# Optimization experiments

Measured on AMD Instinct MI355X. Metric: run time of the kernel, lower is better.

## Reference

```python
import jax, jax.numpy as jnp
from jax import lax
import numpy as np

DIM = 768
NUM_HEADS = 12
HEAD_DIM = DIM // NUM_HEADS
POOL = 8
LAM1_INIT = 0.5
LAM2_INIT = 0.5
EPS = 1e-6


def rmsnorm(x, w):
    # x / (||x||_2 / sqrt(d) + eps) * w
    d = x.shape[-1]
    rms = jnp.sqrt(jnp.sum(x * x, axis=-1, keepdims=True)) / jnp.sqrt(jnp.asarray(d, x.dtype))
    return x / (rms + EPS) * w


def setup_inputs() -> dict:
    key = jax.random.key(0)
    ks = jax.random.split(key, 10)
    B, H, W = 32, 32, 32
    N = H * W
    x = jax.random.normal(ks[0], (B, N, DIM), dtype=jnp.float32)
    Wqkv = jax.random.normal(ks[1], (3 * DIM, DIM), dtype=jnp.float32) * 0.02
    Wproj = jax.random.normal(ks[2], (DIM, DIM), dtype=jnp.float32) * 0.02
    bproj = jnp.zeros((DIM,), dtype=jnp.float32)
    Wpos = jax.random.normal(ks[3], (HEAD_DIM, HEAD_DIM), dtype=jnp.float32) * 0.02
    Wneg = jax.random.normal(ks[4], (HEAD_DIM, HEAD_DIM), dtype=jnp.float32) * 0.02
    conv_w = jax.random.normal(ks[5], (HEAD_DIM, 1, 3, 3), dtype=jnp.float32) * 0.1  # depthwise OIHW
    lam1 = jnp.asarray(LAM1_INIT, dtype=jnp.float32)
    lam2 = jnp.asarray(LAM2_INIT, dtype=jnp.float32)
    norm1_w = jnp.ones((HEAD_DIM,), dtype=jnp.float32)
    norm2_w = jnp.ones((HEAD_DIM,), dtype=jnp.float32)
    return {"x": x, "Wqkv": Wqkv, "Wproj": Wproj, "bproj": bproj, "Wpos": Wpos,
            "Wneg": Wneg, "conv_w": conv_w, "lam1": lam1, "lam2": lam2,
            "norm1_w": norm1_w, "norm2_w": norm2_w, "H": H, "W": W}


def reference(x, Wqkv, Wproj, bproj, Wpos, Wneg, conv_w, lam1, lam2, norm1_w, norm2_w, H, W):
    B, N, C = x.shape
    h, hd, p = NUM_HEADS, HEAD_DIM, POOL
    scale = hd ** -0.5
    # qkv projection -> [3, B, h, N, hd]
    qkv = (x @ Wqkv.T).reshape(B, N, 3, h, hd).transpose(2, 0, 3, 1, 4)
    q, k, v = qkv[0], qkv[1], qkv[2]
    # depthwise conv + GELU on q in spatial form
    q2 = q.reshape(B, h, H, W, hd).transpose(0, 1, 4, 2, 3).reshape(B * h, hd, H, W)
    qe = lax.conv_general_dilated(q2, conv_w, window_strides=(1, 1), padding='SAME',
                                  feature_group_count=hd,
                                  dimension_numbers=('NCHW', 'OIHW', 'NCHW'))
    qe = jax.nn.gelu(qe, approximate=False)
    # adaptive avg pool to (p, p): exact since H % p == 0
    qp = qe.reshape(B * h, hd, p, H // p, p, W // p).mean(axis=(3, 5))
    t_base = qp.reshape(B, h, hd, p, p).transpose(0, 1, 3, 4, 2).reshape(B, h, p * p, hd)
    # dynamic e+/e- embeddings from global query
    gq = q.mean(axis=2)  # [B, h, hd]
    t_pos = t_base + (gq @ Wpos.T)[:, :, None, :]
    t_neg = t_base + (gq @ Wneg.T)[:, :, None, :]
    # stage 1: pooled contrast tokens attend to k/v
    attn_pos = jax.nn.softmax(jnp.einsum('bhmd,bhnd->bhmn', t_pos, k) * scale, axis=-1)
    v_hat_pos = attn_pos @ v  # [B, h, p*p, hd]
    attn_neg = jax.nn.softmax(jnp.einsum('bhmd,bhnd->bhmn', t_neg, k) * scale, axis=-1)
    v_hat_neg = attn_neg @ v
    v_contrast = rmsnorm(v_hat_pos - lam1 * v_hat_neg, norm1_w) * (1.0 - LAM1_INIT)
    # stage 2: q attends to contrast tokens
    attn1 = jax.nn.softmax(jnp.einsum('bhnd,bhmd->bhnm', q, t_pos) * scale, axis=-1)
    attn2 = jax.nn.softmax(jnp.einsum('bhnd,bhmd->bhnm', q, t_neg) * scale, axis=-1)
    out_patch = (attn1 - lam2 * attn2) @ v_contrast  # [B, h, N, hd]
    out_patch = rmsnorm(out_patch, norm2_w) * (1.0 - LAM2_INIT)
    out_patch = out_patch.transpose(0, 2, 1, 3).reshape(B, N, C)
    out = out_patch @ Wproj.T + bproj
    return out
```

## Files before the change

kernel.cpp:

```cpp
#include <hip/hip_runtime.h>
#include <hip/hip_bf16.h>


typedef __attribute__((ext_vector_type(8))) short short8;
typedef __attribute__((ext_vector_type(4))) short bf16x4;
typedef __attribute__((ext_vector_type(4))) float f32x4;

#define DEV static __device__ __forceinline__

DEV unsigned short f2bf(float f) {
  unsigned int b; __builtin_memcpy(&b, &f, 4);
  unsigned int r = (b + 0x7FFFu + ((b >> 16) & 1u)) >> 16;
  return (unsigned short)r;
}
DEV float bf2f(unsigned short u) {
  unsigned int b = ((unsigned int)u) << 16;
  float f; __builtin_memcpy(&f, &b, 4);
  return f;
}

DEV void gload16(const unsigned short* g, unsigned short* l) {
  __builtin_amdgcn_global_load_lds(
      (const __attribute__((address_space(1))) unsigned int*)g,
      (__attribute__((address_space(3))) unsigned int*)l, 16, 0, 0);
}

DEV void bar() {
  asm volatile("" ::: "memory");
  __builtin_amdgcn_s_barrier();
  asm volatile("" ::: "memory");
}
DEV void wait_vm4() { asm volatile("s_waitcnt vmcnt(4)" ::: "memory"); __builtin_amdgcn_sched_barrier(0); }
DEV void wait_vm0() { asm volatile("s_waitcnt vmcnt(0)" ::: "memory"); __builtin_amdgcn_sched_barrier(0); }
DEV void wait_lgkm0() { asm volatile("s_waitcnt lgkmcnt(0)" ::: "memory"); __builtin_amdgcn_sched_barrier(0); }

constexpr size_t SZ_QKV = (size_t)32 * 12 * 1024 * 64 * 2;
constexpr size_t OFF_Q   = 0;
constexpr size_t OFF_K   = OFF_Q + SZ_QKV;
constexpr size_t OFF_VT  = OFF_K + SZ_QKV;
constexpr size_t OFF_TPB = OFF_VT + SZ_QKV;
constexpr size_t OFF_TNB = OFF_TPB + 3145728;
constexpr size_t OFF_VCT = OFF_TNB + 3145728;
constexpr size_t OFF_OP  = OFF_VCT + 6291456;
constexpr size_t OFF_XB  = OFF_OP + SZ_QKV;
constexpr size_t OFF_WQ  = OFF_XB + SZ_QKV;
constexpr size_t OFF_WP  = OFF_WQ + 3538944;
constexpr size_t OFF_EP  = OFF_WP + 1179648;
constexpr size_t OFF_EN  = OFF_EP + 98304;

__global__ __launch_bounds__(256) void cast3_kernel(const float* __restrict__ x,
    const float* __restrict__ wq, const float* __restrict__ wp,
    unsigned short* __restrict__ xd, unsigned short* __restrict__ wqd,
    unsigned short* __restrict__ wpd) {
  const int i = blockIdx.x * 256 + threadIdx.x;
  const float* src; unsigned short* dst; int off;
  if (i < 6291456) { src = x; dst = xd; off = i; }
  else if (i < 6733824) { src = wq; dst = wqd; off = i - 6291456; }
  else { src = wp; dst = wpd; off = i - 6733824; }
  float4 v = reinterpret_cast<const float4*>(src)[off];
  ushort4 o;
  o.x = f2bf(v.x); o.y = f2bf(v.y); o.z = f2bf(v.z); o.w = f2bf(v.w);
  reinterpret_cast<ushort4*>(dst)[off] = o;
}

DEV void stage_ht(const unsigned short* __restrict__ G, unsigned short* shbase,
                  int grow0, int k0, int htrow0, int w, int lane) {
  const int rl = lane >> 3;
  const int ck = (lane & 7) ^ rl;
  const unsigned short* s0 = G + (size_t)(grow0 + htrow0 + w * 16 + rl) * 768 + k0 + ck * 8;
  gload16(s0, shbase + (htrow0 + w * 16) * 64);
  gload16(s0 + (size_t)8 * 768, shbase + (htrow0 + w * 16 + 8) * 64);
}

__global__ __launch_bounds__(512, 2) void gemm_qkv_kernel(const unsigned short* __restrict__ A,
    const unsigned short* __restrict__ Bm, unsigned short* __restrict__ q,
    unsigned short* __restrict__ k, unsigned short* __restrict__ vt) {
  __shared__ __align__(16) unsigned short sh[65536];
  const int t = threadIdx.x;
  const int lane = t & 63;
  const int w = t >> 6;
  const int wm = w >> 2, wn = w & 3;
  const int l = lane & 15, g = lane >> 4;
  const int id = blockIdx.x;
  const int swz = (id & 7) * 144 + (id >> 3);
  const int rt = swz / 9, ct = swz % 9;
  const int row0 = rt * 256, col0 = ct * 256;

  f32x4 acc[8][4];
#pragma unroll
  for (int i = 0; i < 8; ++i)
#pragma unroll
    for (int j = 0; j < 4; ++j) acc[i][j] = (f32x4){0.f, 0.f, 0.f, 0.f};

  stage_ht(A, sh, row0, 0, 0, w, lane);
  stage_ht(A, sh, row0, 0, 128, w, lane);
  stage_ht(Bm, sh + 32768, col0, 0, 0, w, lane);
  stage_ht(Bm, sh + 32768, col0, 0, 128, w, lane);
  stage_ht(Bm, sh + 32768 + 16384, col0, 64, 0, w, lane);
  stage_ht(Bm, sh + 32768 + 16384, col0, 64, 128, w, lane);
  wait_vm4();
  bar();

  for (int m = 0; m < 12; ++m) {
    const int d = m & 1;
    const unsigned short* Ab = sh + d * 16384;
    const unsigned short* Bb = sh + 32768 + d * 16384;
    short8 af[4][2], bf0[2][2], bf1[2][2];
#pragma unroll
    for (int mt = 0; mt < 4; ++mt)
#pragma unroll
      for (int kc = 0; kc < 2; ++kc) {
        const int r = wm * 128 + mt * 16 + l;
        af[mt][kc] = *reinterpret_cast<const short8*>(Ab + r * 64 + (((kc << 2) | g) ^ (r & 7)) * 8);
      }
#pragma unroll
    for (int nt = 0; nt < 2; ++nt)
#pragma unroll
      for (int kc = 0; kc < 2; ++kc) {
        const int r = wn * 64 + nt * 16 + l;
        bf0[nt][kc] = *reinterpret_cast<const short8*>(Bb + r * 64 + (((kc << 2) | g) ^ (r & 7)) * 8);
      }
    if (m + 1 < 12) stage_ht(A, sh + (d ^ 1) * 16384, row0, (m + 1) * 64, 0, w, lane);
    bar();
    __builtin_amdgcn_s_setprio(1);
#pragma unroll
    for (int kc = 0; kc < 2; ++kc)
#pragma unroll
      for (int mt = 0; mt < 4; ++mt)
#pragma unroll
        for (int nt = 0; nt < 2; ++nt)
          acc[mt][nt] = __builtin_amdgcn_mfma_f32_16x16x32_bf16(af[mt][kc], bf0[nt][kc], acc[mt][nt], 0, 0, 0);
    __builtin_amdgcn_s_setprio(0);
    bar();
#pragma unroll
    for (int nt = 0; nt < 2; ++nt)
#pragma unroll
      for (int kc = 0; kc < 2; ++kc) {
        const int r = wn * 64 + 32 + nt * 16 + l;
        bf1[nt][kc] = *reinterpret_cast<const short8*>(Bb + r * 64 + (((kc << 2) | g) ^ (r & 7)) * 8);
      }
    if (m + 1 < 12) stage_ht(A, sh + (d ^ 1) * 16384, row0, (m + 1) * 64, 128, w, lane);
    bar();
    __builtin_amdgcn_s_setprio(1);
#pragma unroll
    for (int kc = 0; kc < 2; ++kc)
#pragma unroll
      for (int mt = 0; mt < 4; ++mt)
#pragma unroll
        for (int nt = 0; nt < 2; ++nt)
          acc[mt][2 + nt] = __builtin_amdgcn_mfma_f32_16x16x32_bf16(af[mt][kc], bf1[nt][kc], acc[mt][2 + nt], 0, 0, 0);
    __builtin_amdgcn_s_setprio(0);
    bar();
#pragma unroll
    for (int mt = 0; mt < 4; ++mt)
#pragma unroll
      for (int kc = 0; kc < 2; ++kc) {
        const int r = wm * 128 + 64 + mt * 16 + l;
        af[mt][kc] = *reinterpret_cast<const short8*>(Ab + r * 64 + (((kc << 2) | g) ^ (r & 7)) * 8);
      }
    if (m + 2 < 12) stage_ht(Bm, sh + 32768 + d * 16384, col0, (m + 2) * 64, 0, w, lane);
    bar();
    __builtin_amdgcn_s_setprio(1);
#pragma unroll
    for (int kc = 0; kc < 2; ++kc)
#pragma unroll
      for (int mt = 0; mt < 4; ++mt)
#pragma unroll
        for (int nt = 0; nt < 2; ++nt)
          acc[4 + mt][2 + nt] = __builtin_amdgcn_mfma_f32_16x16x32_bf16(af[mt][kc], bf1[nt][kc], acc[4 + mt][2 + nt], 0, 0, 0);
    __builtin_amdgcn_s_setprio(0);
    bar();
    if (m + 2 < 12) stage_ht(Bm, sh + 32768 + d * 16384, col0, (m + 2) * 64, 128, w, lane);
    bar();
    __builtin_amdgcn_s_setprio(1);
#pragma unroll
    for (int kc = 0; kc < 2; ++kc)
#pragma unroll
      for (int mt = 0; mt < 4; ++mt)
#pragma unroll
        for (int nt = 0; nt < 2; ++nt)
          acc[4 + mt][nt] = __builtin_amdgcn_mfma_f32_16x16x32_bf16(af[mt][kc], bf0[nt][kc], acc[4 + mt][nt], 0, 0, 0);
    __builtin_amdgcn_s_setprio(0);
    if (m < 11) {
      if (m == 10) wait_vm0(); else wait_vm4();
    }
    bar();
  }

  const int s_ = ct / 3;
  if (s_ == 2) {
#pragma unroll
    for (int ni = 0; ni < 4; ++ni) {
      const int colg = (ct % 3) * 256 + wn * 64 + ni * 16 + l;
      const int head = colg >> 6, dd = colg & 63;
#pragma unroll
      for (int mi = 0; mi < 8; ++mi) {
        const int row = row0 + wm * 128 + mi * 16 + (g << 2);
        const int b = row >> 10, n = row & 1023;
        ushort4 pk;
        pk.x = f2bf(acc[mi][ni][0]); pk.y = f2bf(acc[mi][ni][1]);
        pk.z = f2bf(acc[mi][ni][2]); pk.w = f2bf(acc[mi][ni][3]);
        *reinterpret_cast<ushort4*>(vt + ((((size_t)b * 12 + head) * 64 + dd) << 10) + n) = pk;
      }
    }
  } else {
    unsigned short* dst = (s_ == 0) ? q : k;
#pragma unroll
    for (int ni = 0; ni < 4; ++ni) {
      const int colg = (ct % 3) * 256 + wn * 64 + ni * 16 + l;
      const int head = colg >> 6, dd = colg & 63;
#pragma unroll
      for (int mi = 0; mi < 8; ++mi) {
#pragma unroll
        for (int r = 0; r < 4; ++r) {
          const int row = row0 + wm * 128 + mi * 16 + (g << 2) + r;
          const int b = row >> 10, n = row & 1023;
          dst[(((size_t)b * 12 + head) * 1024 + n) * 64 + dd] = f2bf(acc[mi][ni][r]);
        }
      }
    }
  }
}

__global__ __launch_bounds__(256) void gq_embed_kernel(const unsigned short* __restrict__ qg,
    const float* __restrict__ Wpos, const float* __restrict__ Wneg,
    float* __restrict__ ep, float* __restrict__ en) {
  const int bh = blockIdx.x;
  const unsigned short* qp = qg + (size_t)bh * 65536;
  __shared__ float red2[32][64];
  __shared__ float gq_s[64];
  const int t = threadIdx.x;
  const int c8 = (t & 7) << 3;
  const int part = t >> 3;
  float s[8] = {0.f, 0.f, 0.f, 0.f, 0.f, 0.f, 0.f, 0.f};
  for (int i = 0; i < 32; ++i) {
    const short8 v = *reinterpret_cast<const short8*>(qp + (size_t)(part * 32 + i) * 64 + c8);
#pragma unroll
    for (int j = 0; j < 8; ++j) s[j] += bf2f((unsigned short)v[j]);
  }
#pragma unroll
  for (int j = 0; j < 8; ++j) red2[part][c8 + j] = s[j];
  __syncthreads();
  if (t < 64) {
    float s2 = 0.f;
    for (int p = 0; p < 32; ++p) s2 += red2[p][t];
    gq_s[t] = s2 * (1.0f / 1024.0f);
  }
  __syncthreads();
  if (t < 128) {
    const int d2 = t & 63;
    const float* Wm = (t < 64) ? Wpos : Wneg;
    float e = 0.f;
    for (int dd = 0; dd < 64; ++dd) e += gq_s[dd] * Wm[d2 * 64 + dd];
    (t < 64 ? ep : en)[bh * 64 + d2] = e;
  }
}

__global__ __launch_bounds__(256) void conv_pool_kernel(const unsigned short* __restrict__ qg,
    const float* __restrict__ conv_w, const float* __restrict__ ep,
    const float* __restrict__ en, unsigned short* __restrict__ t_pos,
    unsigned short* __restrict__ t_neg) {
  const int bh = blockIdx.x;
  const int quad = blockIdx.y;
  const unsigned short* qp = qg + (size_t)bh * 65536;
  __shared__ float pool_s[16][64];
  const int t = threadIdx.x;
  const int dg = t & 7, sp = t >> 3;
  const int d0 = dg << 3;
  float cw[3][3][8];
#pragma unroll
  for (int ky = 0; ky < 3; ++ky)
#pragma unroll
    for (int kx = 0; kx < 3; ++kx)
#pragma unroll
      for (int j = 0; j < 8; ++j)
        cw[ky][kx][j] = conv_w[(d0 + j) * 9 + ky * 3 + kx];
#pragma unroll
  for (int pyl = 0; pyl < 2; ++pyl) {
    float win[8] = {0.f, 0.f, 0.f, 0.f, 0.f, 0.f, 0.f, 0.f};
#pragma unroll
    for (int iy = 0; iy < 4; ++iy) {
      const int y = quad * 8 + pyl * 4 + iy;
      float a[8] = {0.f, 0.f, 0.f, 0.f, 0.f, 0.f, 0.f, 0.f};
#pragma unroll
      for (int ky = 0; ky < 3; ++ky) {
        const int yy = y + ky - 1;
        if (yy < 0 || yy > 31) continue;
#pragma unroll
        for (int kx = 0; kx < 3; ++kx) {
          const int xx = sp + kx - 1;
          if (xx < 0 || xx > 31) continue;
          const short8 v = *reinterpret_cast<const short8*>(qp + (size_t)(yy * 32 + xx) * 64 + d0);
#pragma unroll
          for (int j = 0; j < 8; ++j) a[j] += bf2f((unsigned short)v[j]) * cw[ky][kx][j];
        }
      }
#pragma unroll
      for (int j = 0; j < 8; ++j)
        win[j] += 0.5f * a[j] * (1.0f + erff(a[j] * 0.70710678118654752440f));
    }
#pragma unroll
    for (int j = 0; j < 8; ++j) {
      win[j] += __shfl_xor(win[j], 8);
      win[j] += __shfl_xor(win[j], 16);
    }
    if ((sp & 3) == 0) {
      const int px = sp >> 2;
#pragma unroll
      for (int j = 0; j < 8; ++j) pool_s[pyl * 8 + px][d0 + j] = win[j];
    }
  }
  __syncthreads();
#pragma unroll
  for (int i = 0; i < 4; ++i) {
    const int idx = i * 256 + t;
    const int m = idx >> 6, dd = idx & 63;
    const int mg = quad * 16 + m;
    const float base = pool_s[m][dd] * (1.0f / 16.0f);
    t_pos[(size_t)bh * 4096 + mg * 64 + dd] = f2bf(base + ep[bh * 64 + dd]);
    t_neg[(size_t)bh * 4096 + mg * 64 + dd] = f2bf(base + en[bh * 64 + dd]);
  }
}

__global__ __launch_bounds__(256) void stage1_kernel(const unsigned short* __restrict__ kg,
    const unsigned short* __restrict__ vtg, const unsigned short* __restrict__ tpb,
    const unsigned short* __restrict__ tnb, const float* __restrict__ lam1p,
    const float* __restrict__ norm1_w, unsigned short* __restrict__ vct) {
  const int bh = blockIdx.x;
  __shared__ __align__(16) unsigned short Ks[2][4096];
  __shared__ __align__(16) unsigned short Vts[2][4096];
  const int t = threadIdx.x;
  const int lane = t & 63;
  const int w = t >> 6;
  const int l = lane & 15, g = lane >> 4;
  const size_t kbase = (size_t)bh * 65536;
  const int rl = lane >> 3, ck = (lane & 7) ^ rl;

  short8 tf[2][2];
#pragma unroll
  for (int h = 0; h < 2; ++h) {
    tf[0][h] = *reinterpret_cast<const short8*>(tpb + (size_t)bh * 4096 + (w * 16 + l) * 64 + h * 32 + g * 8);
    tf[1][h] = *reinterpret_cast<const short8*>(tnb + (size_t)bh * 4096 + (w * 16 + l) * 64 + h * 32 + g * 8);
  }
  auto stageKV = [&](int buf, int n0) {
    const unsigned short* ksrc = kg + kbase + (size_t)(n0 + w * 16 + rl) * 64 + ck * 8;
    gload16(ksrc, &Ks[buf][(w * 16) * 64]);
    gload16(ksrc + (size_t)8 * 64, &Ks[buf][(w * 16 + 8) * 64]);
    const unsigned short* vsrc = vtg + kbase + (size_t)(w * 16 + rl) * 1024 + n0 + ck * 8;
    gload16(vsrc, &Vts[buf][(w * 16) * 64]);
    gload16(vsrc + (size_t)8 * 1024, &Vts[buf][(w * 16 + 8) * 64]);
  };
  stageKV(0, 0);
  __syncthreads();

  float Mo[2] = {-1e30f, -1e30f}, Lo[2] = {0.f, 0.f};
  f32x4 acc[2][4];
#pragma unroll
  for (int pp = 0; pp < 2; ++pp)
#pragma unroll
    for (int dt = 0; dt < 4; ++dt) acc[pp][dt] = (f32x4){0.f, 0.f, 0.f, 0.f};

  for (int it = 0; it < 16; ++it) {
    const int buf = it & 1;
    if (it < 15) stageKV(buf ^ 1, (it + 1) * 64);
    short8 kf[4][2];
#pragma unroll
    for (int tile = 0; tile < 4; ++tile)
#pragma unroll
      for (int h = 0; h < 2; ++h) {
        const int R = tile * 16 + l;
        kf[tile][h] = *reinterpret_cast<const short8*>(&Ks[buf][R * 64 + ((((h << 2) | g)) ^ (l & 7)) * 8]);
      }
    bf16x4 pf[2][4];
#pragma unroll
    for (int pp = 0; pp < 2; ++pp) {
      f32x4 s[4];
#pragma unroll
      for (int tile = 0; tile < 4; ++tile) {
        s[tile] = (f32x4){0.f, 0.f, 0.f, 0.f};
#pragma unroll
        for (int h = 0; h < 2; ++h)
          s[tile] = __builtin_amdgcn_mfma_f32_16x16x32_bf16(kf[tile][h], tf[pp][h], s[tile], 0, 0, 0);
      }
      float p[4][4];
      float tmax = -1e30f;
#pragma unroll
      for (int tile = 0; tile < 4; ++tile)
#pragma unroll
        for (int r = 0; r < 4; ++r) {
          const float v = s[tile][r] * 0.125f;
          p[tile][r] = v;
          tmax = fmaxf(tmax, v);
        }
      tmax = fmaxf(tmax, __shfl_xor(tmax, 16));
      tmax = fmaxf(tmax, __shfl_xor(tmax, 32));
      const float nm = fmaxf(Mo[pp], tmax);
      const float al = __expf(Mo[pp] - nm);
      Mo[pp] = nm;
      float ps = 0.f;
#pragma unroll
      for (int tile = 0; tile < 4; ++tile)
#pragma unroll
        for (int r = 0; r < 4; ++r) {
          const float e = __expf(p[tile][r] - nm);
          p[tile][r] = e;
          ps += e;
        }
      ps += __shfl_xor(ps, 16);
      ps += __shfl_xor(ps, 32);
      Lo[pp] = Lo[pp] * al + ps;
#pragma unroll
      for (int tile = 0; tile < 4; ++tile) {
        bf16x4 pk;
        pk[0] = (short)f2bf(p[tile][0]); pk[1] = (short)f2bf(p[tile][1]);
        pk[2] = (short)f2bf(p[tile][2]); pk[3] = (short)f2bf(p[tile][3]);
        pf[pp][tile] = pk;
      }
      float ar[4];
#pragma unroll
      for (int r = 0; r < 4; ++r) ar[r] = __shfl(al, 4 * g + r);
#pragma unroll
      for (int dt = 0; dt < 4; ++dt)
#pragma unroll
        for (int r = 0; r < 4; ++r) acc[pp][dt][r] *= ar[r];
    }
#pragma unroll
    for (int tile = 0; tile < 4; ++tile)
#pragma unroll
      for (int dt = 0; dt < 4; ++dt) {
        const int R = dt * 16 + l;
        const bf16x4 vf = *reinterpret_cast<const bf16x4*>(
            &Vts[buf][R * 64 + (((2 * tile + (g >> 1)) ^ (l & 7)) * 8) + (g & 1) * 4]);
        acc[0][dt] = __builtin_amdgcn_mfma_f32_16x16x16bf16_1k(pf[0][tile], vf, acc[0][dt], 0, 0, 0);
        acc[1][dt] = __builtin_amdgcn_mfma_f32_16x16x16bf16_1k(pf[1][tile], vf, acc[1][dt], 0, 0, 0);
      }
    __syncthreads();
  }
  const float inv0 = 1.f / Lo[0], inv1 = 1.f / Lo[1];
  float i1r[4], i2r[4];
#pragma unroll
  for (int r = 0; r < 4; ++r) {
    i1r[r] = __shfl(inv0, 4 * g + r);
    i2r[r] = __shfl(inv1, 4 * g + r);
  }
  const float lam1 = lam1p[0];
  float od[4][4], ss[4] = {0.f, 0.f, 0.f, 0.f};
#pragma unroll
  for (int dt = 0; dt < 4; ++dt)
#pragma unroll
    for (int r = 0; r < 4; ++r) {
      const float v = acc[0][dt][r] * i1r[r] - lam1 * (acc[1][dt][r] * i2r[r]);
      od[dt][r] = v;
      ss[r] += v * v;
    }
#pragma unroll
  for (int r = 0; r < 4; ++r) {
    ss[r] += __shfl_xor(ss[r], 1);
    ss[r] += __shfl_xor(ss[r], 2);
    ss[r] += __shfl_xor(ss[r], 4);
    ss[r] += __shfl_xor(ss[r], 8);
  }
  float sc[4];
#pragma unroll
  for (int r = 0; r < 4; ++r) sc[r] = 0.5f / (sqrtf(ss[r]) * 0.125f + 1e-6f);
  const int mb = w * 16 + 4 * g;
#pragma unroll
  for (int dt = 0; dt < 4; ++dt) {
    const int dd = dt * 16 + l;
    const float nw = norm1_w[dd];
    ushort4 pk;
    pk.x = f2bf(od[dt][0] * sc[0] * nw);
    pk.y = f2bf(od[dt][1] * sc[1] * nw);
    pk.z = f2bf(od[dt][2] * sc[2] * nw);
    pk.w = f2bf(od[dt][3] * sc[3] * nw);
    *reinterpret_cast<ushort4*>(vct + (size_t)bh * 4096 + dd * 64 + mb) = pk;
  }
}

__global__ __launch_bounds__(256) void stage2_kernel(const unsigned short* __restrict__ qg,
    const unsigned short* __restrict__ tpb, const unsigned short* __restrict__ tnb,
    const unsigned short* __restrict__ vctg, const float* __restrict__ lam2p,
    const float* __restrict__ norm2_w, unsigned short* __restrict__ opb) {
  const int bh = blockIdx.x;
  const int q0 = blockIdx.y * 256;
  __shared__ unsigned short tp[64 * 72], tn[64 * 72], Vc[64 * 72];
  __shared__ unsigned short Qs[256 * 72];
  const int t = threadIdx.x;
  const int lane = t & 63;
  const int w = t >> 6;
  const int l = lane & 15, g = lane >> 4;
  for (int L = t; L < 512; L += 256) {
    const int r = L >> 3, c = (L & 7) << 3;
    *reinterpret_cast<short8*>(tp + r * 72 + c) =
        *reinterpret_cast<const short8*>(tpb + (size_t)bh * 4096 + r * 64 + c);
    *reinterpret_cast<short8*>(tn + r * 72 + c) =
        *reinterpret_cast<const short8*>(tnb + (size_t)bh * 4096 + r * 64 + c);
    *reinterpret_cast<short8*>(Vc + r * 72 + c) =
        *reinterpret_cast<const short8*>(vctg + (size_t)bh * 4096 + r * 64 + c);
  }
  for (int L = t; L < 2048; L += 256) {
    const int r = L >> 3, c = (L & 7) << 3;
    *reinterpret_cast<short8*>(Qs + r * 72 + c) =
        *reinterpret_cast<const short8*>(qg + (size_t)bh * 65536 + (size_t)(q0 + r) * 64 + c);
  }
  __syncthreads();
  bf16x4 vcf[4][4];
#pragma unroll
  for (int tile = 0; tile < 4; ++tile)
#pragma unroll
    for (int dt = 0; dt < 4; ++dt)
      vcf[tile][dt] = *reinterpret_cast<const bf16x4*>(Vc + (dt * 16 + l) * 72 + tile * 16 + g * 4);
  const float lam2 = lam2p[0];
  const int b = bh / 12, head = bh % 12;
  float nw[4];
#pragma unroll
  for (int dt = 0; dt < 4; ++dt) nw[dt] = norm2_w[dt * 16 + l];

  for (int s = 0; s < 4; ++s) {
    const int rrow = (w * 4 + s) * 16;
    short8 qf[2];
#pragma unroll
    for (int h = 0; h < 2; ++h)
      qf[h] = *reinterpret_cast<const short8*>(Qs + (rrow + l) * 72 + h * 32 + g * 8);
    bf16x4 pf[2][4];
#pragma unroll
    for (int pp = 0; pp < 2; ++pp) {
      const unsigned short* tm = pp ? tn : tp;
      f32x4 sv[4];
#pragma unroll
      for (int tile = 0; tile < 4; ++tile) {
        sv[tile] = (f32x4){0.f, 0.f, 0.f, 0.f};
#pragma unroll
        for (int h = 0; h < 2; ++h) {
          const short8 tfb = *reinterpret_cast<const short8*>(tm + (tile * 16 + l) * 72 + h * 32 + g * 8);
          sv[tile] = __builtin_amdgcn_mfma_f32_16x16x32_bf16(tfb, qf[h], sv[tile], 0, 0, 0);
        }
      }
      float p[4][4];
      float lmax = -1e30f;
#pragma unroll
      for (int tile = 0; tile < 4; ++tile)
#pragma unroll
        for (int r = 0; r < 4; ++r) {
          const float v = sv[tile][r] * 0.125f;
          p[tile][r] = v;
          lmax = fmaxf(lmax, v);
        }
      lmax = fmaxf(lmax, __shfl_xor(lmax, 16));
      lmax = fmaxf(lmax, __shfl_xor(lmax, 32));
      float ps = 0.f;
#pragma unroll
      for (int tile = 0; tile < 4; ++tile)
#pragma unroll
        for (int r = 0; r < 4; ++r) {
          const float e = __expf(p[tile][r] - lmax);
          p[tile][r] = e;
          ps += e;
        }
      ps += __shfl_xor(ps, 16);
      ps += __shfl_xor(ps, 32);
      const float inv = 1.f / ps;
#pragma unroll
      for (int tile = 0; tile < 4; ++tile) {
        bf16x4 pk;
        pk[0] = (short)f2bf(p[tile][0] * inv); pk[1] = (short)f2bf(p[tile][1] * inv);
        pk[2] = (short)f2bf(p[tile][2] * inv); pk[3] = (short)f2bf(p[tile][3] * inv);
        pf[pp][tile] = pk;
      }
    }
    f32x4 a1[4], a2[4];
#pragma unroll
    for (int dt = 0; dt < 4; ++dt) {
      a1[dt] = (f32x4){0.f, 0.f, 0.f, 0.f};
      a2[dt] = (f32x4){0.f, 0.f, 0.f, 0.f};
    }
#pragma unroll
    for (int tile = 0; tile < 4; ++tile)
#pragma unroll
      for (int dt = 0; dt < 4; ++dt) {
        a1[dt] = __builtin_amdgcn_mfma_f32_16x16x16bf16_1k(pf[0][tile], vcf[tile][dt], a1[dt], 0, 0, 0);
        a2[dt] = __builtin_amdgcn_mfma_f32_16x16x16bf16_1k(pf[1][tile], vcf[tile][dt], a2[dt], 0, 0, 0);
      }
    float od[4][4], ss[4] = {0.f, 0.f, 0.f, 0.f};
#pragma unroll
    for (int dt = 0; dt < 4; ++dt)
#pragma unroll
      for (int r = 0; r < 4; ++r) {
        const float v = a1[dt][r] - lam2 * a2[dt][r];
        od[dt][r] = v;
        ss[r] += v * v;
      }
#pragma unroll
    for (int r = 0; r < 4; ++r) {
      ss[r] += __shfl_xor(ss[r], 1);
      ss[r] += __shfl_xor(ss[r], 2);
      ss[r] += __shfl_xor(ss[r], 4);
      ss[r] += __shfl_xor(ss[r], 8);
    }
    float sc[4];
#pragma unroll
    for (int r = 0; r < 4; ++r) sc[r] = 0.5f / (sqrtf(ss[r]) * 0.125f + 1e-6f);
    const size_t ob = ((size_t)b * 1024 + q0 + rrow + 4 * g) * 768 + head * 64;
#pragma unroll
    for (int dt = 0; dt < 4; ++dt) {
#pragma unroll
      for (int r = 0; r < 4; ++r)
        opb[ob + (size_t)r * 768 + dt * 16 + l] = f2bf(od[dt][r] * sc[r] * nw[dt]);
    }
  }
}

__global__ __launch_bounds__(512, 2) void gemm_proj_kernel(const unsigned short* __restrict__ A,
    const unsigned short* __restrict__ Bm, const float* __restrict__ bias,
    float* __restrict__ out) {
  __shared__ __align__(16) unsigned short sh[49152];
  const int t = threadIdx.x;
  const int lane = t & 63;
  const int w = t >> 6;
  const int wm = w >> 2, wn = w & 3;
  const int l = lane & 15, g = lane >> 4;
  const int id = blockIdx.x;
  const int swz = (id & 7) * 96 + (id >> 3);
  const int rt = swz / 3, ct = swz % 3;
  const int row0 = rt * 128, col0 = ct * 256;

  f32x4 acc[4][4];
#pragma unroll
  for (int i = 0; i < 4; ++i)
#pragma unroll
    for (int j = 0; j < 4; ++j) acc[i][j] = (f32x4){0.f, 0.f, 0.f, 0.f};

  stage_ht(A, sh, row0, 0, 0, w, lane);
  stage_ht(Bm, sh + 16384, col0, 0, 0, w, lane);
  stage_ht(Bm, sh + 16384, col0, 0, 128, w, lane);
  stage_ht(Bm, sh + 32768, col0, 64, 0, w, lane);
  stage_ht(Bm, sh + 32768, col0, 64, 128, w, lane);
  wait_vm4();
  bar();

  for (int m = 0; m < 12; ++m) {
    const int d = m & 1;
    const unsigned short* Ab = sh + d * 8192;
    const unsigned short* Bb = sh + 16384 + d * 16384;
    short8 af[4][2], bfv[4][2];
#pragma unroll
    for (int mt = 0; mt < 4; ++mt)
#pragma unroll
      for (int kc = 0; kc < 2; ++kc) {
        const int r = wm * 64 + mt * 16 + l;
        af[mt][kc] = *reinterpret_cast<const short8*>(Ab + r * 64 + (((kc << 2) | g) ^ (r & 7)) * 8);
      }
#pragma unroll
    for (int nt = 0; nt < 2; ++nt)
#pragma unroll
      for (int kc = 0; kc < 2; ++kc) {
        const int r = wn * 64 + nt * 16 + l;
        bfv[nt][kc] = *reinterpret_cast<const short8*>(Bb + r * 64 + (((kc << 2) | g) ^ (r & 7)) * 8);
      }
    if (m + 1 < 12) stage_ht(A, sh + (d ^ 1) * 8192, row0, (m + 1) * 64, 0, w, lane);
    bar();
    __builtin_amdgcn_s_setprio(1);
#pragma unroll
    for (int kc = 0; kc < 2; ++kc)
#pragma unroll
      for (int mt = 0; mt < 4; ++mt)
#pragma unroll
        for (int nt = 0; nt < 2; ++nt)
          acc[mt][nt] = __builtin_amdgcn_mfma_f32_16x16x32_bf16(af[mt][kc], bfv[nt][kc], acc[mt][nt], 0, 0, 0);
    __builtin_amdgcn_s_setprio(0);
    bar();
#pragma unroll
    for (int nt = 2; nt < 4; ++nt)
#pragma unroll
      for (int kc = 0; kc < 2; ++kc) {
        const int r = wn * 64 + nt * 16 + l;
        bfv[nt][kc] = *reinterpret_cast<const short8*>(Bb + r * 64 + (((kc << 2) | g) ^ (r & 7)) * 8);
      }
    wait_lgkm0();
    bar();
    if (m + 2 < 12) {
      stage_ht(Bm, sh + 16384 + d * 16384, col0, (m + 2) * 64, 0, w, lane);
      stage_ht(Bm, sh + 16384 + d * 16384, col0, (m + 2) * 64, 128, w, lane);
    }
    __builtin_amdgcn_s_setprio(1);
#pragma unroll
    for (int kc = 0; kc < 2; ++kc)
#pragma unroll
      for (int mt = 0; mt < 4; ++mt)
#pragma unroll
        for (int nt = 2; nt < 4; ++nt)
          acc[mt][nt] = __builtin_amdgcn_mfma_f32_16x16x32_bf16(af[mt][kc], bfv[nt][kc], acc[mt][nt], 0, 0, 0);
    __builtin_amdgcn_s_setprio(0);
    if (m < 11) {
      if (m == 10) wait_vm0(); else wait_vm4();
    }
    bar();
  }
#pragma unroll
  for (int ni = 0; ni < 4; ++ni) {
    const int colg = ct * 256 + wn * 64 + ni * 16 + l;
    const float bv = bias[colg];
#pragma unroll
    for (int mi = 0; mi < 4; ++mi)
#pragma unroll
      for (int r = 0; r < 4; ++r) {
        const int row = row0 + wm * 64 + mi * 16 + (g << 2) + r;
        out[(size_t)row * 768 + colg] = acc[mi][ni][r] + bv;
      }
  }
}

extern "C" void kernel_launch(void* const* d_in, const int* in_sizes, int n_in,
                              void* d_out, int out_size, void* d_ws, size_t ws_size,
                              hipStream_t stream) {
  (void)in_sizes; (void)n_in; (void)out_size; (void)ws_size;
  const float* x       = (const float*)d_in[0];
  const float* Wqkv    = (const float*)d_in[1];
  const float* Wproj   = (const float*)d_in[2];
  const float* bproj   = (const float*)d_in[3];
  const float* Wpos    = (const float*)d_in[4];
  const float* Wneg    = (const float*)d_in[5];
  const float* conv_w  = (const float*)d_in[6];
  const float* lam1    = (const float*)d_in[7];
  const float* lam2    = (const float*)d_in[8];
  const float* norm1_w = (const float*)d_in[9];
  const float* norm2_w = (const float*)d_in[10];
  float* out = (float*)d_out;
  char* ws = (char*)d_ws;
  unsigned short* qb   = (unsigned short*)(ws + OFF_Q);
  unsigned short* kb   = (unsigned short*)(ws + OFF_K);
  unsigned short* vtb  = (unsigned short*)(ws + OFF_VT);
  unsigned short* tpbb = (unsigned short*)(ws + OFF_TPB);
  unsigned short* tnbb = (unsigned short*)(ws + OFF_TNB);
  unsigned short* vctb = (unsigned short*)(ws + OFF_VCT);
  unsigned short* opb  = (unsigned short*)(ws + OFF_OP);
  unsigned short* xb   = (unsigned short*)(ws + OFF_XB);
  unsigned short* wqb  = (unsigned short*)(ws + OFF_WQ);
  unsigned short* wpb  = (unsigned short*)(ws + OFF_WP);
  float* epb           = (float*)(ws + OFF_EP);
  float* enb           = (float*)(ws + OFF_EN);

  cast3_kernel<<<dim3(26880), dim3(256), 0, stream>>>(x, Wqkv, Wproj, xb, wqb, wpb);
  gemm_qkv_kernel<<<dim3(1152), dim3(512), 0, stream>>>(xb, wqb, qb, kb, vtb);
  gq_embed_kernel<<<dim3(384), dim3(256), 0, stream>>>(qb, Wpos, Wneg, epb, enb);
  conv_pool_kernel<<<dim3(384, 4), dim3(256), 0, stream>>>(qb, conv_w, epb, enb, tpbb, tnbb);
  stage1_kernel<<<dim3(384), dim3(256), 0, stream>>>(kb, vtb, tpbb, tnbb, lam1, norm1_w, vctb);
  stage2_kernel<<<dim3(384, 4), dim3(256), 0, stream>>>(qb, tpbb, tnbb, vctb, lam2, norm2_w, opb);
  gemm_proj_kernel<<<dim3(768), dim3(512), 0, stream>>>(opb, wpb, bproj, out);
}
```

Before: 391.5 us.

## Fuse stage1/stage2 attention and fold global-query mean into QKV GEMM epilogue

The global query mean is now accumulated by atomics in the QKV GEMM epilogue, with the buffer zeroed in the cast kernel, which removes the separate gq_embed kernel. The Wpos/Wneg embedding is computed inside conv_pool. Stage1 and stage2 are fused into one kernel per (batch, head), so v_contrast stays in LDS instead of going through global memory, and Q rows are streamed with register prefetch. In exchange, stage2 work drops from 1536 blocks to 384 blocks that each loop over all 1024 rows, which lowers parallelism. The float atomics also make the summation order nondeterministic.

```diff
diff --git a/kernel.cpp b/kernel.cpp
--- a/kernel.cpp
+++ b/kernel.cpp
@@ -40,19 +40,18 @@
 constexpr size_t OFF_VT  = OFF_K + SZ_QKV;
 constexpr size_t OFF_TPB = OFF_VT + SZ_QKV;
 constexpr size_t OFF_TNB = OFF_TPB + 3145728;
-constexpr size_t OFF_VCT = OFF_TNB + 3145728;
-constexpr size_t OFF_OP  = OFF_VCT + 6291456;
+constexpr size_t OFF_OP  = OFF_TNB + 3145728;
 constexpr size_t OFF_XB  = OFF_OP + SZ_QKV;
 constexpr size_t OFF_WQ  = OFF_XB + SZ_QKV;
 constexpr size_t OFF_WP  = OFF_WQ + 3538944;
-constexpr size_t OFF_EP  = OFF_WP + 1179648;
-constexpr size_t OFF_EN  = OFF_EP + 98304;
+constexpr size_t OFF_GQ  = OFF_WP + 1179648;
 
 __global__ __launch_bounds__(256) void cast3_kernel(const float* __restrict__ x,
     const float* __restrict__ wq, const float* __restrict__ wp,
     unsigned short* __restrict__ xd, unsigned short* __restrict__ wqd,
-    unsigned short* __restrict__ wpd) {
+    unsigned short* __restrict__ wpd, float* __restrict__ gqs) {
   const int i = blockIdx.x * 256 + threadIdx.x;
+  if (i < 24576) gqs[i] = 0.f;
   const float* src; unsigned short* dst; int off;
   if (i < 6291456) { src = x; dst = xd; off = i; }
   else if (i < 6733824) { src = wq; dst = wqd; off = i - 6291456; }
@@ -74,7 +73,8 @@
 
 __global__ __launch_bounds__(512, 2) void gemm_qkv_kernel(const unsigned short* __restrict__ A,
     const unsigned short* __restrict__ Bm, unsigned short* __restrict__ q,
-    unsigned short* __restrict__ k, unsigned short* __restrict__ vt) {
+    unsigned short* __restrict__ k, unsigned short* __restrict__ vt,
+    float* __restrict__ gqs) {
   __shared__ __align__(16) unsigned short sh[65536];
   const int t = threadIdx.x;
   const int lane = t & 63;
@@ -219,52 +219,43 @@
         }
       }
     }
-  }
-}
-
-__global__ __launch_bounds__(256) void gq_embed_kernel(const unsigned short* __restrict__ qg,
-    const float* __restrict__ Wpos, const float* __restrict__ Wneg,
-    float* __restrict__ ep, float* __restrict__ en) {
+    if (s_ == 0) {
+      const int b = row0 >> 10;
+#pragma unroll
+      for (int ni = 0; ni < 4; ++ni) {
+        const int colg = ct * 256 + wn * 64 + ni * 16 + l;
+        const int head = colg >> 6, dd = colg & 63;
+        float gs = 0.f;
+#pragma unroll
+        for (int mi = 0; mi < 8; ++mi)
+#pragma unroll
+          for (int r = 0; r < 4; ++r) gs += acc[mi][ni][r];
+        gs += __shfl_xor(gs, 16);
+        gs += __shfl_xor(gs, 32);
+        if (g == 0) atomicAdd(&gqs[((size_t)b * 12 + head) * 64 + dd], gs);
+      }
+    }
+  }
+}
+
+__global__ __launch_bounds__(256) void conv_pool_kernel(const unsigned short* __restrict__ qg,
+    const float* __restrict__ conv_w, const float* __restrict__ Wpos,
+    const float* __restrict__ Wneg, const float* __restrict__ gqs,
+    unsigned short* __restrict__ t_pos, unsigned short* __restrict__ t_neg) {
   const int bh = blockIdx.x;
+  const int quad = blockIdx.y;
   const unsigned short* qp = qg + (size_t)bh * 65536;
-  __shared__ float red2[32][64];
-  __shared__ float gq_s[64];
+  __shared__ float pool_s[16][64];
+  __shared__ float ep_s[64], en_s[64];
   const int t = threadIdx.x;
-  const int c8 = (t & 7) << 3;
-  const int part = t >> 3;
-  float s[8] = {0.f, 0.f, 0.f, 0.f, 0.f, 0.f, 0.f, 0.f};
-  for (int i = 0; i < 32; ++i) {
-    const short8 v = *reinterpret_cast<const short8*>(qp + (size_t)(part * 32 + i) * 64 + c8);
-#pragma unroll
-    for (int j = 0; j < 8; ++j) s[j] += bf2f((unsigned short)v[j]);
-  }
-#pragma unroll
-  for (int j = 0; j < 8; ++j) red2[part][c8 + j] = s[j];
-  __syncthreads();
-  if (t < 64) {
-    float s2 = 0.f;
-    for (int p = 0; p < 32; ++p) s2 += red2[p][t];
-    gq_s[t] = s2 * (1.0f / 1024.0f);
-  }
-  __syncthreads();
   if (t < 128) {
     const int d2 = t & 63;
     const float* Wm = (t < 64) ? Wpos : Wneg;
     float e = 0.f;
-    for (int dd = 0; dd < 64; ++dd) e += gq_s[dd] * Wm[d2 * 64 + dd];
-    (t < 64 ? ep : en)[bh * 64 + d2] = e;
-  }
-}
-
-__global__ __launch_bounds__(256) void conv_pool_kernel(const unsigned short* __restrict__ qg,
-    const float* __restrict__ conv_w, const float* __restrict__ ep,
-    const float* __restrict__ en, unsigned short* __restrict__ t_pos,
-    unsigned short* __restrict__ t_neg) {
-  const int bh = blockIdx.x;
-  const int quad = blockIdx.y;
-  const unsigned short* qp = qg + (size_t)bh * 65536;
-  __shared__ float pool_s[16][64];
-  const int t = threadIdx.x;
+    for (int dd = 0; dd < 64; ++dd)
+      e += gqs[bh * 64 + dd] * (1.0f / 1024.0f) * Wm[d2 * 64 + dd];
+    (t < 64 ? ep_s : en_s)[d2] = e;
+  }
   const int dg = t & 7, sp = t >> 3;
   const int d0 = dg << 3;
   float cw[3][3][8];
@@ -317,16 +308,19 @@
     const int m = idx >> 6, dd = idx & 63;
     const int mg = quad * 16 + m;
     const float base = pool_s[m][dd] * (1.0f / 16.0f);
-    t_pos[(size_t)bh * 4096 + mg * 64 + dd] = f2bf(base + ep[bh * 64 + dd]);
-    t_neg[(size_t)bh * 4096 + mg * 64 + dd] = f2bf(base + en[bh * 64 + dd]);
-  }
-}
-
-__global__ __launch_bounds__(256) void stage1_kernel(const unsigned short* __restrict__ kg,
-    const unsigned short* __restrict__ vtg, const unsigned short* __restrict__ tpb,
-    const unsigned short* __restrict__ tnb, const float* __restrict__ lam1p,
-    const float* __restrict__ norm1_w, unsigned short* __restrict__ vct) {
+    t_pos[(size_t)bh * 4096 + mg * 64 + dd] = f2bf(base + ep_s[dd]);
+    t_neg[(size_t)bh * 4096 + mg * 64 + dd] = f2bf(base + en_s[dd]);
+  }
+}
+
+__global__ __launch_bounds__(256) void stage12_kernel(const unsigned short* __restrict__ kg,
+    const unsigned short* __restrict__ vtg, const unsigned short* __restrict__ qg,
+    const unsigned short* __restrict__ tpb, const unsigned short* __restrict__ tnb,
+    const float* __restrict__ lam1p, const float* __restrict__ norm1_w,
+    const float* __restrict__ lam2p, const float* __restrict__ norm2_w,
+    unsigned short* __restrict__ opb) {
   const int bh = blockIdx.x;
+  __shared__ unsigned short tp[64 * 72], tn[64 * 72], Vc[64 * 72];
   __shared__ __align__(16) unsigned short Ks[2][4096];
   __shared__ __align__(16) unsigned short Vts[2][4096];
   const int t = threadIdx.x;
@@ -336,11 +330,12 @@
   const size_t kbase = (size_t)bh * 65536;
   const int rl = lane >> 3, ck = (lane & 7) ^ rl;
 
-  short8 tf[2][2];
-#pragma unroll
-  for (int h = 0; h < 2; ++h) {
-    tf[0][h] = *reinterpret_cast<const short8*>(tpb + (size_t)bh * 4096 + (w * 16 + l) * 64 + h * 32 + g * 8);
-    tf[1][h] = *reinterpret_cast<const short8*>(tnb + (size_t)bh * 4096 + (w * 16 + l) * 64 + h * 32 + g * 8);
+  for (int L = t; L < 512; L += 256) {
+    const int r = L >> 3, c = (L & 7) << 3;
+    *reinterpret_cast<short8*>(tp + r * 72 + c) =
+        *reinterpret_cast<const short8*>(tpb + (size_t)bh * 4096 + r * 64 + c);
+    *reinterpret_cast<short8*>(tn + r * 72 + c) =
+        *reinterpret_cast<const short8*>(tnb + (size_t)bh * 4096 + r * 64 + c);
   }
   auto stageKV = [&](int buf, int n0) {
     const unsigned short* ksrc = kg + kbase + (size_t)(n0 + w * 16 + rl) * 64 + ck * 8;
@@ -353,6 +348,12 @@
   stageKV(0, 0);
   __syncthreads();
 
+  short8 tf[2][2];
+#pragma unroll
+  for (int h = 0; h < 2; ++h) {
+    tf[0][h] = *reinterpret_cast<const short8*>(tp + (w * 16 + l) * 72 + h * 32 + g * 8);
+    tf[1][h] = *reinterpret_cast<const short8*>(tn + (w * 16 + l) * 72 + h * 32 + g * 8);
+  }
   float Mo[2] = {-1e30f, -1e30f}, Lo[2] = {0.f, 0.f};
   f32x4 acc[2][4];
 #pragma unroll
@@ -436,74 +437,49 @@
       }
     __syncthreads();
   }
-  const float inv0 = 1.f / Lo[0], inv1 = 1.f / Lo[1];
-  float i1r[4], i2r[4];
-#pragma unroll
-  for (int r = 0; r < 4; ++r) {
-    i1r[r] = __shfl(inv0, 4 * g + r);
-    i2r[r] = __shfl(inv1, 4 * g + r);
-  }
-  const float lam1 = lam1p[0];
-  float od[4][4], ss[4] = {0.f, 0.f, 0.f, 0.f};
-#pragma unroll
-  for (int dt = 0; dt < 4; ++dt)
+  {
+    const float inv0 = 1.f / Lo[0], inv1 = 1.f / Lo[1];
+    float i1r[4], i2r[4];
 #pragma unroll
     for (int r = 0; r < 4; ++r) {
-      const float v = acc[0][dt][r] * i1r[r] - lam1 * (acc[1][dt][r] * i2r[r]);
-      od[dt][r] = v;
-      ss[r] += v * v;
-    }
-#pragma unroll
-  for (int r = 0; r < 4; ++r) {
-    ss[r] += __shfl_xor(ss[r], 1);
-    ss[r] += __shfl_xor(ss[r], 2);
-    ss[r] += __shfl_xor(ss[r], 4);
-    ss[r] += __shfl_xor(ss[r], 8);
-  }
-  float sc[4];
-#pragma unroll
-  for (int r = 0; r < 4; ++r) sc[r] = 0.5f / (sqrtf(ss[r]) * 0.125f + 1e-6f);
-  const int mb = w * 16 + 4 * g;
-#pragma unroll
-  for (int dt = 0; dt < 4; ++dt) {
-    const int dd = dt * 16 + l;
-    const float nw = norm1_w[dd];
-    ushort4 pk;
-    pk.x = f2bf(od[dt][0] * sc[0] * nw);
-    pk.y = f2bf(od[dt][1] * sc[1] * nw);
-    pk.z = f2bf(od[dt][2] * sc[2] * nw);
-    pk.w = f2bf(od[dt][3] * sc[3] * nw);
-    *reinterpret_cast<ushort4*>(vct + (size_t)bh * 4096 + dd * 64 + mb) = pk;
-  }
-}
-
-__global__ __launch_bounds__(256) void stage2_kernel(const unsigned short* __restrict__ qg,
-    const unsigned short* __restrict__ tpb, const unsigned short* __restrict__ tnb,
-    const unsigned short* __restrict__ vctg, const float* __restrict__ lam2p,
-    const float* __restrict__ norm2_w, unsigned short* __restrict__ opb) {
-  const int bh = blockIdx.x;
-  const int q0 = blockIdx.y * 256;
-  __shared__ unsigned short tp[64 * 72], tn[64 * 72], Vc[64 * 72];
-  __shared__ unsigned short Qs[256 * 72];
-  const int t = threadIdx.x;
-  const int lane = t & 63;
-  const int w = t >> 6;
-  const int l = lane & 15, g = lane >> 4;
-  for (int L = t; L < 512; L += 256) {
-    const int r = L >> 3, c = (L & 7) << 3;
-    *reinterpret_cast<short8*>(tp + r * 72 + c) =
-        *reinterpret_cast<const short8*>(tpb + (size_t)bh * 4096 + r * 64 + c);
-    *reinterpret_cast<short8*>(tn + r * 72 + c) =
-        *reinterpret_cast<const short8*>(tnb + (size_t)bh * 4096 + r * 64 + c);
-    *reinterpret_cast<short8*>(Vc + r * 72 + c) =
-        *reinterpret_cast<const short8*>(vctg + (size_t)bh * 4096 + r * 64 + c);
-  }
-  for (int L = t; L < 2048; L += 256) {
-    const int r = L >> 3, c = (L & 7) << 3;
-    *reinterpret_cast<short8*>(Qs + r * 72 + c) =
-        *reinterpret_cast<const short8*>(qg + (size_t)bh * 65536 + (size_t)(q0 + r) * 64 + c);
+      i1r[r] = __shfl(inv0, 4 * g + r);
+      i2r[r] = __shfl(inv1, 4 * g + r);
+    }
+    const float lam1 = lam1p[0];
+    float od[4][4], ss[4] = {0.f, 0.f, 0.f, 0.f};
+#pragma unroll
+    for (int dt = 0; dt < 4; ++dt)
+#pragma unroll
+      for (int r = 0; r < 4; ++r) {
+        const float v = acc[0][dt][r] * i1r[r] - lam1 * (acc[1][dt][r] * i2r[r]);
+        od[dt][r] = v;
+        ss[r] += v * v;
+      }
+#pragma unroll
+    for (int r = 0; r < 4; ++r) {
+      ss[r] += __shfl_xor(ss[r], 1);
+      ss[r] += __shfl_xor(ss[r], 2);
+      ss[r] += __shfl_xor(ss[r], 4);
+      ss[r] += __shfl_xor(ss[r], 8);
+    }
+    float sc[4];
+#pragma unroll
+    for (int r = 0; r < 4; ++r) sc[r] = 0.5f / (sqrtf(ss[r]) * 0.125f + 1e-6f);
+    const int mb = w * 16 + 4 * g;
+#pragma unroll
+    for (int dt = 0; dt < 4; ++dt) {
+      const int dd = dt * 16 + l;
+      const float nw = norm1_w[dd];
+      ushort4 pk;
+      pk.x = f2bf(od[dt][0] * sc[0] * nw);
+      pk.y = f2bf(od[dt][1] * sc[1] * nw);
+      pk.z = f2bf(od[dt][2] * sc[2] * nw);
+      pk.w = f2bf(od[dt][3] * sc[3] * nw);
+      *reinterpret_cast<ushort4*>(Vc + dd * 72 + mb) = pk;
+    }
   }
   __syncthreads();
+
   bf16x4 vcf[4][4];
 #pragma unroll
   for (int tile = 0; tile < 4; ++tile)
@@ -512,16 +488,20 @@
       vcf[tile][dt] = *reinterpret_cast<const bf16x4*>(Vc + (dt * 16 + l) * 72 + tile * 16 + g * 4);
   const float lam2 = lam2p[0];
   const int b = bh / 12, head = bh % 12;
-  float nw[4];
-#pragma unroll
-  for (int dt = 0; dt < 4; ++dt) nw[dt] = norm2_w[dt * 16 + l];
-
-  for (int s = 0; s < 4; ++s) {
-    const int rrow = (w * 4 + s) * 16;
-    short8 qf[2];
-#pragma unroll
-    for (int h = 0; h < 2; ++h)
-      qf[h] = *reinterpret_cast<const short8*>(Qs + (rrow + l) * 72 + h * 32 + g * 8);
+  float nw2[4];
+#pragma unroll
+  for (int dt = 0; dt < 4; ++dt) nw2[dt] = norm2_w[dt * 16 + l];
+  const unsigned short* qrow = qg + kbase;
+
+  short8 qf0 = *reinterpret_cast<const short8*>(qrow + (size_t)(w * 256 + l) * 64 + g * 8);
+  short8 qf1 = *reinterpret_cast<const short8*>(qrow + (size_t)(w * 256 + l) * 64 + 32 + g * 8);
+  for (int s = 0; s < 16; ++s) {
+    const int rbase = w * 256 + s * 16;
+    short8 qn0, qn1;
+    if (s < 15) {
+      qn0 = *reinterpret_cast<const short8*>(qrow + (size_t)(rbase + 16 + l) * 64 + g * 8);
+      qn1 = *reinterpret_cast<const short8*>(qrow + (size_t)(rbase + 16 + l) * 64 + 32 + g * 8);
+    }
     bf16x4 pf[2][4];
 #pragma unroll
     for (int pp = 0; pp < 2; ++pp) {
@@ -530,11 +510,10 @@
 #pragma unroll
       for (int tile = 0; tile < 4; ++tile) {
         sv[tile] = (f32x4){0.f, 0.f, 0.f, 0.f};
-#pragma unroll
-        for (int h = 0; h < 2; ++h) {
-          const short8 tfb = *reinterpret_cast<const short8*>(tm + (tile * 16 + l) * 72 + h * 32 + g * 8);
-          sv[tile] = __builtin_amdgcn_mfma_f32_16x16x32_bf16(tfb, qf[h], sv[tile], 0, 0, 0);
-        }
+        const short8 tfb0 = *reinterpret_cast<const short8*>(tm + (tile * 16 + l) * 72 + g * 8);
+        const short8 tfb1 = *reinterpret_cast<const short8*>(tm + (tile * 16 + l) * 72 + 32 + g * 8);
+        sv[tile] = __builtin_amdgcn_mfma_f32_16x16x32_bf16(tfb0, qf0, sv[tile], 0, 0, 0);
+        sv[tile] = __builtin_amdgcn_mfma_f32_16x16x32_bf16(tfb1, qf1, sv[tile], 0, 0, 0);
       }
       float p[4][4];
       float lmax = -1e30f;
@@ -600,13 +579,14 @@
     float sc[4];
 #pragma unroll
     for (int r = 0; r < 4; ++r) sc[r] = 0.5f / (sqrtf(ss[r]) * 0.125f + 1e-6f);
-    const size_t ob = ((size_t)b * 1024 + q0 + rrow + 4 * g) * 768 + head * 64;
+    const size_t ob = ((size_t)b * 1024 + rbase + 4 * g) * 768 + head * 64;
 #pragma unroll
     for (int dt = 0; dt < 4; ++dt) {
 #pragma unroll
       for (int r = 0; r < 4; ++r)
-        opb[ob + (size_t)r * 768 + dt * 16 + l] = f2bf(od[dt][r] * sc[r] * nw[dt]);
-    }
+        opb[ob + (size_t)r * 768 + dt * 16 + l] = f2bf(od[dt][r] * sc[r] * nw2[dt]);
+    }
+    if (s < 15) { qf0 = qn0; qf1 = qn1; }
   }
 }
 
@@ -732,19 +712,15 @@
   unsigned short* vtb  = (unsigned short*)(ws + OFF_VT);
   unsigned short* tpbb = (unsigned short*)(ws + OFF_TPB);
   unsigned short* tnbb = (unsigned short*)(ws + OFF_TNB);
-  unsigned short* vctb = (unsigned short*)(ws + OFF_VCT);
   unsigned short* opb  = (unsigned short*)(ws + OFF_OP);
   unsigned short* xb   = (unsigned short*)(ws + OFF_XB);
   unsigned short* wqb  = (unsigned short*)(ws + OFF_WQ);
   unsigned short* wpb  = (unsigned short*)(ws + OFF_WP);
-  float* epb           = (float*)(ws + OFF_EP);
-  float* enb           = (float*)(ws + OFF_EN);
-
-  cast3_kernel<<<dim3(26880), dim3(256), 0, stream>>>(x, Wqkv, Wproj, xb, wqb, wpb);
-  gemm_qkv_kernel<<<dim3(1152), dim3(512), 0, stream>>>(xb, wqb, qb, kb, vtb);
-  gq_embed_kernel<<<dim3(384), dim3(256), 0, stream>>>(qb, Wpos, Wneg, epb, enb);
-  conv_pool_kernel<<<dim3(384, 4), dim3(256), 0, stream>>>(qb, conv_w, epb, enb, tpbb, tnbb);
-  stage1_kernel<<<dim3(384), dim3(256), 0, stream>>>(kb, vtb, tpbb, tnbb, lam1, norm1_w, vctb);
-  stage2_kernel<<<dim3(384, 4), dim3(256), 0, stream>>>(qb, tpbb, tnbb, vctb, lam2, norm2_w, opb);
+  float* gqsb          = (float*)(ws + OFF_GQ);
+
+  cast3_kernel<<<dim3(26880), dim3(256), 0, stream>>>(x, Wqkv, Wproj, xb, wqb, wpb, gqsb);
+  gemm_qkv_kernel<<<dim3(1152), dim3(512), 0, stream>>>(xb, wqb, qb, kb, vtb, gqsb);
+  conv_pool_kernel<<<dim3(384, 4), dim3(256), 0, stream>>>(qb, conv_w, Wpos, Wneg, gqsb, tpbb, tnbb);
+  stage12_kernel<<<dim3(384), dim3(256), 0, stream>>>(kb, vtb, qb, tpbb, tnbb, lam1, norm1_w, lam2, norm2_w, opb);
   gemm_proj_kernel<<<dim3(768), dim3(512), 0, stream>>>(opb, wpb, bproj, out);
 }
```

Result: no change. 387.6 us (-1.0%).
